# Performance work log

Measured on AMD Instinct MI355X. Metric: run time of the kernel, lower is better.

The kernel has to match this reference:

```python
import jax, jax.numpy as jnp
import numpy as np

DIM = 768
HEAD = 12


def setup_inputs() -> dict:
    key = jax.random.key(0)
    ks = jax.random.split(key, 7)
    B, N, C = 4, 2048, DIM
    s = 0.02
    return {
        "x": jax.random.normal(ks[0], (B, N, C), dtype=jnp.float32),
        "wq": jax.random.normal(ks[1], (C, C), dtype=jnp.float32) * s,
        "bq": jax.random.normal(ks[2], (C,), dtype=jnp.float32) * s,
        "wkv": jax.random.normal(ks[3], (C, 2 * C), dtype=jnp.float32) * s,
        "bkv": jax.random.normal(ks[4], (2 * C,), dtype=jnp.float32) * s,
        "wp": jax.random.normal(ks[5], (C, C), dtype=jnp.float32) * s,
        "bp": jax.random.normal(ks[6], (C,), dtype=jnp.float32) * s,
    }


def reference(x, wq, bq, wkv, bkv, wp, bp):
    B, N, C = x.shape
    H = HEAD
    D = C // H
    scale = D ** -0.5
    # projections
    q = (x @ wq + bq).reshape(B, N, H, D)          # [B,N,H,D]
    kv = (x @ wkv + bkv).reshape(B, N, 2, H, D)
    k = kv[:, :, 0]                                 # [B,N,H,D]
    v = kv[:, :, 1]
    # attention scores [B,H,N,N]
    attn = jnp.einsum('bnhd,bmhd->bhnm', q, k) * scale
    attn = jax.nn.softmax(attn, axis=-1)
    x_atten = jnp.einsum('bhnm,bmhd->bnhd', attn, v).reshape(B, N, C)
    return x_atten @ wp + bp
```

## Files before the change

### kernel.cpp

```cpp
#include <hip/hip_runtime.h>

typedef unsigned short u16;
typedef __attribute__((ext_vector_type(8))) short bf16x8;
typedef __attribute__((ext_vector_type(4))) float f32x4;

#define MFMA(a, b, c) __builtin_amdgcn_mfma_f32_16x16x32_bf16(a, b, c, 0, 0, 0)
#define LOG2E 1.44269504088896340736f

__device__ __forceinline__ u16 f2bf(float f) {
    union { float f; unsigned u; } v; v.f = f;
    unsigned r = v.u + 0x7fffu + ((v.u >> 16) & 1u);
    return (u16)(r >> 16);
}
__device__ __forceinline__ float bf2f(u16 h) {
    union { unsigned u; float f; } v; v.u = ((unsigned)h) << 16;
    return v.f;
}
__device__ __forceinline__ unsigned pkbf(float a, float b) {
    unsigned r;
    asm("v_cvt_pk_bf16_f32 %0, %1, %2" : "=v"(r) : "v"(a), "v"(b));
    return r;
}
__device__ __forceinline__ float ex2(float x) {
#if __has_builtin(__builtin_amdgcn_exp2f)
    return __builtin_amdgcn_exp2f(x);
#else
    return exp2f(x);
#endif
}
__device__ __forceinline__ bf16x8 frag_from(unsigned a, unsigned b, unsigned c, unsigned d) {
    uint4 v; v.x = a; v.y = b; v.z = c; v.w = d;
    return __builtin_bit_cast(bf16x8, v);
}

__device__ __forceinline__ void g2l16(const void* g, void* lds_base) {
    __builtin_amdgcn_global_load_lds(
        (const __attribute__((address_space(1))) unsigned*)(unsigned long long)(uintptr_t)g,
        (__attribute__((address_space(3))) unsigned*)(unsigned)(uintptr_t)lds_base,
        16, 0, 0);
}

__global__ __launch_bounds__(256) void prep_kernel(
    const float* __restrict__ x, const float* __restrict__ wq,
    const float* __restrict__ wkv, const float* __restrict__ wp,
    u16* __restrict__ xb, u16* __restrict__ wtqkv, u16* __restrict__ wtp)
{
    int bz = blockIdx.x;
    int t = threadIdx.x;
    if (bz < 6144) {
        int i = (bz * 256 + t) * 4;
        float4 v = *(const float4*)&x[i];
        uint2 o;
        o.x = pkbf(v.x, v.y);
        o.y = pkbf(v.z, v.w);
        *(uint2*)&xb[i] = o;
        return;
    }
    __shared__ float tile[32][33];
    const float* W; u16* Wt; int cols; int r = bz - 6144;
    if (r < 576)       { W = wq;  Wt = wtqkv;             cols = 768;  }
    else if (r < 1728) { W = wkv; Wt = wtqkv + 768 * 768; cols = 1536; r -= 576; }
    else               { W = wp;  Wt = wtp;               cols = 768;  r -= 1728; }
    int nbx = cols / 32;
    int bx = (r % nbx) * 32, by = (r / nbx) * 32;
    int tx = t & 31, ty = t >> 5;
    for (int i = 0; i < 4; i++)
        tile[ty + 8 * i][tx] = W[(size_t)(by + ty + 8 * i) * cols + bx + tx];
    __syncthreads();
    for (int i = 0; i < 4; i++)
        Wt[(size_t)(bx + ty + 8 * i) * 768 + by + tx] = f2bf(tile[tx][ty + 8 * i]);
}

__global__ __launch_bounds__(256, 4) void gemm128(
    const u16* __restrict__ A, const u16* __restrict__ Bt,
    const float* __restrict__ bias0, const float* __restrict__ bias1, int bsplit,
    u16* __restrict__ outB, u16* __restrict__ vtg, int M, int N, int K)
{
    __shared__ __align__(16) u16 smem[17408];
    u16* As = smem;
    u16* Bs = smem + 8192;
    u16* Cs = smem;

    int gid = blockIdx.x;
    int bmi = ((gid & 7) << 3) | ((gid >> 3) & 7);
    int bni = gid >> 6;
    int bm = bmi * 128, bn = bni * 128;

    int t = threadIdx.x;
    int w = t >> 6, l = t & 63, q4 = l >> 4, lm = l & 15, lm7 = l & 7;
    int wm = (w >> 1) * 64, wn = (w & 1) * 64;

    f32x4 acc[4][4];
    for (int i = 0; i < 4; i++) for (int j = 0; j < 4; j++) acc[i][j] = (f32x4){0, 0, 0, 0};

    int srow = l >> 3;
    int schunk = (l & 7) ^ srow;

    for (int kt = 0; kt < K; kt += 64) {
        for (int p = 0; p < 4; p++) {
            int row = p * 32 + w * 8 + srow;
            g2l16(&A [(size_t)(bm + row) * K + kt + schunk * 8], &As[(p * 32 + w * 8) * 64]);
            g2l16(&Bt[(size_t)(bn + row) * K + kt + schunk * 8], &Bs[(p * 32 + w * 8) * 64]);
        }
        __syncthreads();
        for (int kc = 0; kc < 2; kc++) {
            bf16x8 a[4], b[4];
            for (int i = 0; i < 4; i++)
                a[i] = *(const bf16x8*)&As[(wm + 16 * i + lm) * 64 + ((4 * kc + q4) ^ lm7) * 8];
            for (int j = 0; j < 4; j++)
                b[j] = *(const bf16x8*)&Bs[(wn + 16 * j + lm) * 64 + ((4 * kc + q4) ^ lm7) * 8];
            for (int i = 0; i < 4; i++)
                for (int j = 0; j < 4; j++)
                    acc[i][j] = MFMA(a[i], b[j], acc[i][j]);
        }
        __syncthreads();
    }

    if (bn < 1536) {
        for (int i = 0; i < 4; i++)
            for (int j = 0; j < 4; j++) {
                int col = bn + wn + 16 * j + lm;
                float bv = (col < bsplit) ? bias0[col] : bias1[col - bsplit];
                for (int r = 0; r < 4; r++)
                    Cs[(wm + 16 * i + 4 * q4 + r) * 132 + wn + 16 * j + lm] =
                        f2bf(acc[i][j][r] + bv);
            }
        __syncthreads();
        int row = t >> 1, c0 = (t & 1) * 8;
        for (int s = 0; s < 8; s++)
            *(uint4*)&outB[(size_t)(bm + row) * N + bn + c0 + s * 16] =
                *(const uint4*)&Cs[row * 132 + c0 + s * 16];
    } else {
        for (int i = 0; i < 4; i++)
            for (int j = 0; j < 4; j++) {
                int cl = wn + 16 * j + lm;
                float bv = bias1[bn + cl - bsplit];
                uint2 pk;
                pk.x = pkbf(acc[i][j][0] + bv, acc[i][j][1] + bv);
                pk.y = pkbf(acc[i][j][2] + bv, acc[i][j][3] + bv);
                *(uint2*)&Cs[cl * 132 + wm + 16 * i + 4 * q4] = pk;
            }
        __syncthreads();
        int c = t >> 1, half = t & 1;
        int d = c & 63, hloc = c >> 6;
        int b = bm >> 11;
        int bh = b * 12 + ((bn - 1536) >> 6) + hloc;
        size_t rowoff = ((size_t)bh * 64 + d) * 2048 + (bm & 2047) + half * 64;
        const u16* base = &Cs[c * 132 + half * 64];
        for (int oct = 0; oct < 8; oct++) {
            int n0 = 32 * (oct >> 2) + 4 * (oct & 3);
            uint2 lo = *(const uint2*)&base[n0];
            uint2 hi = *(const uint2*)&base[n0 + 16];
            uint4 o; o.x = lo.x; o.y = lo.y; o.z = hi.x; o.w = hi.y;
            *(uint4*)&vtg[rowoff + oct * 8] = o;
        }
    }
}

__global__ __launch_bounds__(256, 4) void gemm_n64(
    const u16* __restrict__ A, const u16* __restrict__ Bt,
    const float* __restrict__ bias, float* __restrict__ outF, int M, int N, int K)
{
    __shared__ __align__(16) u16 smem[12288];
    u16* As = smem;
    u16* Bs = smem + 8192;
    float* Cf = (float*)smem;

    int gid = blockIdx.x;
    int bmi = ((gid & 7) << 3) | ((gid >> 3) & 7);
    int bni = gid >> 6;
    int bm = bmi * 128, bn = bni * 64;

    int t = threadIdx.x;
    int w = t >> 6, l = t & 63, q4 = l >> 4, lm = l & 15, lm7 = l & 7;
    int wm = (w >> 1) * 64, wn = (w & 1) * 32;

    f32x4 acc[4][2];
    for (int i = 0; i < 4; i++) for (int j = 0; j < 2; j++) acc[i][j] = (f32x4){0, 0, 0, 0};

    int srow = l >> 3;
    int schunk = (l & 7) ^ srow;

    for (int kt = 0; kt < K; kt += 64) {
        for (int p = 0; p < 4; p++) {
            int row = p * 32 + w * 8 + srow;
            g2l16(&A[(size_t)(bm + row) * K + kt + schunk * 8], &As[(p * 32 + w * 8) * 64]);
        }
        for (int p = 0; p < 2; p++) {
            int row = p * 32 + w * 8 + srow;
            g2l16(&Bt[(size_t)(bn + row) * K + kt + schunk * 8], &Bs[(p * 32 + w * 8) * 64]);
        }
        __syncthreads();
        for (int kc = 0; kc < 2; kc++) {
            bf16x8 a[4], b[2];
            for (int i = 0; i < 4; i++)
                a[i] = *(const bf16x8*)&As[(wm + 16 * i + lm) * 64 + ((4 * kc + q4) ^ lm7) * 8];
            for (int j = 0; j < 2; j++)
                b[j] = *(const bf16x8*)&Bs[(wn + 16 * j + lm) * 64 + ((4 * kc + q4) ^ lm7) * 8];
            for (int i = 0; i < 4; i++)
                for (int j = 0; j < 2; j++)
                    acc[i][j] = MFMA(a[i], b[j], acc[i][j]);
        }
        __syncthreads();
    }

    for (int round = 0; round < 2; round++) {
        if (round) __syncthreads();
        if ((w >> 1) == round) {
            for (int i = 0; i < 4; i++)
                for (int j = 0; j < 2; j++) {
                    int cl = wn + 16 * j + lm;
                    float bv = bias[bn + cl];
                    for (int r = 0; r < 4; r++)
                        Cf[(16 * i + 4 * q4 + r) * 68 + cl] = acc[i][j][r] + bv;
                }
        }
        __syncthreads();
        int row = t >> 4, c4 = (t & 15) * 4;
        for (int s = 0; s < 4; s++) {
            int rr = row + s * 16;
            *(float4*)&outF[(size_t)(bm + round * 64 + rr) * N + bn + c4] =
                *(const float4*)&Cf[rr * 68 + c4];
        }
    }
}

__global__ __launch_bounds__(256, 3) void attn_kernel(const u16* __restrict__ qkv,
                                                      const u16* __restrict__ vtg,
                                                      u16* __restrict__ xatt)
{
    __shared__ __align__(16) u16 smem[16384];

    int gid = blockIdx.x;
    int bh = gid % 48, qt = gid / 48;
    int b = bh / 12, h = bh % 12;

    int t = threadIdx.x;
    int w = t >> 6, l = t & 63, q4 = l >> 4, lm = l & 15, lm7 = l & 7;
    int qw = qt * 128 + w * 32;
    size_t rowbase = (size_t)b * 2048;

    int srow = l >> 3;
    int schunk = (l & 7) ^ srow;
    const u16* kp[2];
    const u16* vp[2];
    for (int p = 0; p < 2; p++) {
        int row = w * 16 + p * 8 + srow;
        kp[p] = &qkv[(rowbase + row) * 2304 + 768 + h * 64 + schunk * 8];
        vp[p] = &vtg[((size_t)bh * 64 + row) * 2048 + schunk * 8];
    }

    bf16x8 qf[2][2];
    for (int qi = 0; qi < 2; qi++) {
        size_t row = rowbase + qw + 16 * qi + lm;
        for (int kq = 0; kq < 2; kq++) {
            bf16x8 raw = *(const bf16x8*)&qkv[row * 2304 + h * 64 + kq * 32 + q4 * 8];
            bf16x8 sc;
            for (int j = 0; j < 8; j++) sc[j] = (short)f2bf(bf2f((u16)raw[j]) * (0.125f * LOG2E));
            qf[qi][kq] = sc;
        }
    }

    const bf16x8 ONES = frag_from(0x3F803F80u, 0x3F803F80u, 0x3F803F80u, 0x3F803F80u);

    int offA = lm * 64 + (q4 ^ lm7) * 8;
    int offB = lm * 64 + ((4 | q4) ^ lm7) * 8;

    f32x4 acc[2][4];
    f32x4 acc_l[2];
    for (int qi = 0; qi < 2; qi++) {
        for (int dt = 0; dt < 4; dt++) acc[qi][dt] = (f32x4){0, 0, 0, 0};
        acc_l[qi] = (f32x4){0, 0, 0, 0};
    }

    for (int p = 0; p < 2; p++) {
        g2l16(kp[p], smem + (w * 16 + p * 8) * 64);
        g2l16(vp[p], smem + 8192 + (w * 16 + p * 8) * 64);
    }

    const size_t KSTEP = (size_t)64 * 2304;
    for (int it = 0; it < 32; it++) {
        __syncthreads();
        int buf = it & 1;
        if (it + 1 < 32) {
            int nbuf = buf ^ 1;
            for (int p = 0; p < 2; p++) {
                kp[p] += KSTEP;
                vp[p] += 64;
                g2l16(kp[p], smem + nbuf * 4096 + (w * 16 + p * 8) * 64);
                g2l16(vp[p], smem + 8192 + nbuf * 4096 + (w * 16 + p * 8) * 64);
            }
        }
        const u16* Kb = smem + buf * 4096;
        const u16* Vb = smem + 8192 + buf * 4096;

        f32x4 s[2][4];
        for (int kt2 = 0; kt2 < 4; kt2++) {
            bf16x8 kf0 = *(const bf16x8*)&Kb[kt2 * 1024 + offA];
            bf16x8 kf1 = *(const bf16x8*)&Kb[kt2 * 1024 + offB];
            __builtin_amdgcn_s_setprio(1);
            for (int qi = 0; qi < 2; qi++) {
                f32x4 z = {0, 0, 0, 0};
                z = MFMA(kf0, qf[qi][0], z);
                z = MFMA(kf1, qf[qi][1], z);
                s[qi][kt2] = z;
            }
            __builtin_amdgcn_s_setprio(0);
        }

        bf16x8 vf0[4], vf1[4];
        for (int dt = 0; dt < 4; dt++) {
            vf0[dt] = *(const bf16x8*)&Vb[dt * 1024 + offA];
            vf1[dt] = *(const bf16x8*)&Vb[dt * 1024 + offB];
        }

        for (int qi = 0; qi < 2; qi++) {
            uint2 pk[4];
            for (int kt2 = 0; kt2 < 4; kt2++) {
                float p0 = ex2(s[qi][kt2][0]);
                float p1 = ex2(s[qi][kt2][1]);
                float p2 = ex2(s[qi][kt2][2]);
                float p3 = ex2(s[qi][kt2][3]);
                pk[kt2].x = pkbf(p0, p1);
                pk[kt2].y = pkbf(p2, p3);
            }

            bf16x8 af0 = frag_from(pk[0].x, pk[0].y, pk[1].x, pk[1].y);
            bf16x8 af1 = frag_from(pk[2].x, pk[2].y, pk[3].x, pk[3].y);
            __builtin_amdgcn_s_setprio(1);
            for (int dt = 0; dt < 4; dt++) {
                acc[qi][dt] = MFMA(af0, vf0[dt], acc[qi][dt]);
                acc[qi][dt] = MFMA(af1, vf1[dt], acc[qi][dt]);
            }
            acc_l[qi] = MFMA(af0, ONES, acc_l[qi]);
            acc_l[qi] = MFMA(af1, ONES, acc_l[qi]);
            __builtin_amdgcn_s_setprio(0);
        }
    }

    for (int qi = 0; qi < 2; qi++) {
        float ar[4];
        for (int r = 0; r < 4; r++) ar[r] = 1.0f / acc_l[qi][r];
        for (int dt = 0; dt < 4; dt++)
            for (int r = 0; r < 4; r++) {
                int row = qw + 16 * qi + 4 * q4 + r;
                xatt[(rowbase + row) * 768 + h * 64 + 16 * dt + lm] =
                    f2bf(acc[qi][dt][r] * ar[r]);
            }
    }
}

extern "C" void kernel_launch(void* const* d_in, const int* in_sizes, int n_in,
                              void* d_out, int out_size, void* d_ws, size_t ws_size,
                              hipStream_t stream)
{
    const float* x   = (const float*)d_in[0];
    const float* wq  = (const float*)d_in[1];
    const float* bq  = (const float*)d_in[2];
    const float* wkv = (const float*)d_in[3];
    const float* bkv = (const float*)d_in[4];
    const float* wp  = (const float*)d_in[5];
    const float* bp  = (const float*)d_in[6];
    float* out = (float*)d_out;

    char* ws = (char*)d_ws;
    u16* xb    = (u16*)(ws);
    u16* wtqkv = (u16*)(ws + 12582912);
    u16* wtp   = (u16*)(ws + 16121856);
    u16* qkvb  = (u16*)(ws + 17301504);
    u16* xatt  = (u16*)(ws + 55050240);
    u16* vtg   = (u16*)(ws + 67632128);

    prep_kernel<<<8448, 256, 0, stream>>>(x, wq, wkv, wp, xb, wtqkv, wtp);

    gemm128<<<1152, 256, 0, stream>>>(
        xb, wtqkv, bq, bkv, 768, qkvb, vtg, 8192, 2304, 768);

    attn_kernel<<<768, 256, 0, stream>>>(qkvb, vtg, xatt);

    gemm_n64<<<768, 256, 0, stream>>>(
        xatt, wtp, bp, out, 8192, 768, 768);
}
```

Before: 198.7 us.

## Shrink gemm128 LDS epilogue to two halves, raise occupancy, drop setprio in attention

```diff
diff --git a/kernel.cpp b/kernel.cpp
--- a/kernel.cpp
+++ b/kernel.cpp
@@ -20,6 +20,9 @@
     unsigned r;
     asm("v_cvt_pk_bf16_f32 %0, %1, %2" : "=v"(r) : "v"(a), "v"(b));
     return r;
+}
+__device__ __forceinline__ u16 cvt1bf(float a) {
+    return (u16)pkbf(a, a);
 }
 __device__ __forceinline__ float ex2(float x) {
 #if __has_builtin(__builtin_amdgcn_exp2f)
@@ -71,12 +74,12 @@
         Wt[(size_t)(bx + ty + 8 * i) * 768 + by + tx] = f2bf(tile[tx][ty + 8 * i]);
 }
 
-__global__ __launch_bounds__(256, 4) void gemm128(
+__global__ __launch_bounds__(256, 5) void gemm128(
     const u16* __restrict__ A, const u16* __restrict__ Bt,
     const float* __restrict__ bias0, const float* __restrict__ bias1, int bsplit,
     u16* __restrict__ outB, u16* __restrict__ vtg, int M, int N, int K)
 {
-    __shared__ __align__(16) u16 smem[17408];
+    __shared__ __align__(16) u16 smem[16384];
     u16* As = smem;
     u16* Bs = smem + 8192;
     u16* Cs = smem;
@@ -117,42 +120,54 @@
     }
 
     if (bn < 1536) {
-        for (int i = 0; i < 4; i++)
-            for (int j = 0; j < 4; j++) {
-                int col = bn + wn + 16 * j + lm;
-                float bv = (col < bsplit) ? bias0[col] : bias1[col - bsplit];
-                for (int r = 0; r < 4; r++)
-                    Cs[(wm + 16 * i + 4 * q4 + r) * 132 + wn + 16 * j + lm] =
-                        f2bf(acc[i][j][r] + bv);
-            }
-        __syncthreads();
-        int row = t >> 1, c0 = (t & 1) * 8;
-        for (int s = 0; s < 8; s++)
-            *(uint4*)&outB[(size_t)(bm + row) * N + bn + c0 + s * 16] =
-                *(const uint4*)&Cs[row * 132 + c0 + s * 16];
+        for (int round = 0; round < 2; round++) {
+            if (round) __syncthreads();
+            if ((w >> 1) == round) {
+                for (int i = 0; i < 4; i++)
+                    for (int j = 0; j < 4; j++) {
+                        int col = bn + wn + 16 * j + lm;
+                        float bv = (col < bsplit) ? bias0[col] : bias1[col - bsplit];
+                        for (int r = 0; r < 4; r++) {
+                            float v = acc[i][j][r] + bv;
+                            Cs[(16 * i + 4 * q4 + r) * 132 + wn + 16 * j + lm] = cvt1bf(v);
+                        }
+                    }
+            }
+            __syncthreads();
+            int row = t >> 2, sub = t & 3;
+            for (int s = 0; s < 4; s++)
+                *(uint4*)&outB[(size_t)(bm + round * 64 + row) * N + bn + sub * 8 + s * 32] =
+                    *(const uint4*)&Cs[row * 132 + sub * 8 + s * 32];
+        }
     } else {
-        for (int i = 0; i < 4; i++)
-            for (int j = 0; j < 4; j++) {
-                int cl = wn + 16 * j + lm;
-                float bv = bias1[bn + cl - bsplit];
-                uint2 pk;
-                pk.x = pkbf(acc[i][j][0] + bv, acc[i][j][1] + bv);
-                pk.y = pkbf(acc[i][j][2] + bv, acc[i][j][3] + bv);
-                *(uint2*)&Cs[cl * 132 + wm + 16 * i + 4 * q4] = pk;
-            }
-        __syncthreads();
-        int c = t >> 1, half = t & 1;
-        int d = c & 63, hloc = c >> 6;
+        int cfull = t >> 1, o2 = t & 1;
+        int d = cfull & 63, hloc = cfull >> 6;
         int b = bm >> 11;
         int bh = b * 12 + ((bn - 1536) >> 6) + hloc;
-        size_t rowoff = ((size_t)bh * 64 + d) * 2048 + (bm & 2047) + half * 64;
-        const u16* base = &Cs[c * 132 + half * 64];
-        for (int oct = 0; oct < 8; oct++) {
-            int n0 = 32 * (oct >> 2) + 4 * (oct & 3);
-            uint2 lo = *(const uint2*)&base[n0];
-            uint2 hi = *(const uint2*)&base[n0 + 16];
-            uint4 o; o.x = lo.x; o.y = lo.y; o.z = hi.x; o.w = hi.y;
-            *(uint4*)&vtg[rowoff + oct * 8] = o;
+        for (int round = 0; round < 2; round++) {
+            if (round) __syncthreads();
+            if ((w >> 1) == round) {
+                for (int i = 0; i < 4; i++)
+                    for (int j = 0; j < 4; j++) {
+                        int cl = wn + 16 * j + lm;
+                        float bv = bias1[bn + cl - bsplit];
+                        uint2 pk;
+                        pk.x = pkbf(acc[i][j][0] + bv, acc[i][j][1] + bv);
+                        pk.y = pkbf(acc[i][j][2] + bv, acc[i][j][3] + bv);
+                        *(uint2*)&Cs[cl * 68 + 16 * i + 4 * q4] = pk;
+                    }
+            }
+            __syncthreads();
+            size_t rowoff = ((size_t)bh * 64 + d) * 2048 + (bm & 2047) + round * 64;
+            const u16* base = &Cs[cfull * 68];
+            for (int o = 0; o < 4; o++) {
+                int oct = o2 * 4 + o;
+                int n0 = 32 * (oct >> 2) + 4 * (oct & 3);
+                uint2 lo = *(const uint2*)&base[n0];
+                uint2 hi = *(const uint2*)&base[n0 + 16];
+                uint4 ov; ov.x = lo.x; ov.y = lo.y; ov.z = hi.x; ov.w = hi.y;
+                *(uint4*)&vtg[rowoff + oct * 8] = ov;
+            }
         }
     }
 }
@@ -298,14 +313,12 @@
         for (int kt2 = 0; kt2 < 4; kt2++) {
             bf16x8 kf0 = *(const bf16x8*)&Kb[kt2 * 1024 + offA];
             bf16x8 kf1 = *(const bf16x8*)&Kb[kt2 * 1024 + offB];
-            __builtin_amdgcn_s_setprio(1);
             for (int qi = 0; qi < 2; qi++) {
                 f32x4 z = {0, 0, 0, 0};
                 z = MFMA(kf0, qf[qi][0], z);
                 z = MFMA(kf1, qf[qi][1], z);
                 s[qi][kt2] = z;
             }
-            __builtin_amdgcn_s_setprio(0);
         }
 
         bf16x8 vf0[4], vf1[4];
@@ -327,14 +340,12 @@
 
             bf16x8 af0 = frag_from(pk[0].x, pk[0].y, pk[1].x, pk[1].y);
             bf16x8 af1 = frag_from(pk[2].x, pk[2].y, pk[3].x, pk[3].y);
-            __builtin_amdgcn_s_setprio(1);
             for (int dt = 0; dt < 4; dt++) {
                 acc[qi][dt] = MFMA(af0, vf0[dt], acc[qi][dt]);
                 acc[qi][dt] = MFMA(af1, vf1[dt], acc[qi][dt]);
             }
             acc_l[qi] = MFMA(af0, ONES, acc_l[qi]);
             acc_l[qi] = MFMA(af1, ONES, acc_l[qi]);
-            __builtin_amdgcn_s_setprio(0);
         }
     }
 
```

Measured after the change: 262.0 us. 31.8% more time.
